# Optimization experiments

Measured on AMD Instinct MI355X. Metric: run time of the kernel, lower is better.

Reference implementation:

```python
import jax, jax.numpy as jnp
import numpy as np

B, S, D = 8, 2048, 256
H, DFF, L = 8, 1024, 5
DK = D // H
EPS = 1e-5


def _xavier(key, shape):
    fan_in, fan_out = shape[-2], shape[-1]
    a = jnp.sqrt(6.0 / (fan_in + fan_out))
    return jax.random.uniform(key, shape, jnp.float32, -a, a)


def setup_inputs() -> dict:
    key = jax.random.key(0)
    ks = jax.random.split(key, 12)
    inp = {
        "src": jax.random.normal(ks[0], (B, S, D), jnp.float32),
        "sph": jax.random.normal(ks[1], (B, S, S), jnp.float32),
        # stacked per-layer parameters, leading dim = L
        "Wq": _xavier(ks[2], (L, D, D)), "bq": jnp.zeros((L, D), jnp.float32),
        "Wk": _xavier(ks[3], (L, D, D)), "bk": jnp.zeros((L, D), jnp.float32),
        "Wv": _xavier(ks[4], (L, D, D)), "bv": jnp.zeros((L, D), jnp.float32),
        "Wo": _xavier(ks[5], (L, D, D)), "bo": jnp.zeros((L, D), jnp.float32),
        "W1": _xavier(ks[6], (L, D, DFF)), "b1": jnp.zeros((L, DFF), jnp.float32),
        "W2": _xavier(ks[7], (L, DFF, D)), "b2": jnp.zeros((L, D), jnp.float32),
        "ln1_g": jnp.ones((L, D), jnp.float32), "ln1_b": jnp.zeros((L, D), jnp.float32),
        "ln2_g": jnp.ones((L, D), jnp.float32), "ln2_b": jnp.zeros((L, D), jnp.float32),
    }
    return inp


def _layernorm(x, g, b):
    mu = jnp.mean(x, axis=-1, keepdims=True)
    var = jnp.mean(jnp.square(x - mu), axis=-1, keepdims=True)
    return (x - mu) * jax.lax.rsqrt(var + EPS) * g + b


def _layer(x, sph, Wq, bq, Wk, bk, Wv, bv, Wo, bo, W1, b1, W2, b2, g1, be1, g2, be2):
    # multihead attention with additive sph score bias
    q = (x @ Wq + bq).reshape(B, S, H, DK)
    k = (x @ Wk + bk).reshape(B, S, H, DK)
    v = (x @ Wv + bv).reshape(B, S, H, DK)
    scores = jnp.einsum("bqhd,bkhd->bhqk", q, k) / jnp.sqrt(jnp.float32(DK))
    scores = scores + sph[:, None, :, :]  # bias broadcast over heads
    attn = jax.nn.softmax(scores, axis=-1)
    ctx = jnp.einsum("bhqk,bkhd->bqhd", attn, v).reshape(B, S, D)
    src2 = ctx @ Wo + bo
    x = _layernorm(x + src2, g1, be1)
    # FFN (exact gelu, matching torch F.gelu default)
    h = jax.nn.gelu(x @ W1 + b1, approximate=False)
    src2 = h @ W2 + b2
    x = _layernorm(x + src2, g2, be2)
    return x


def reference(src, sph, Wq, bq, Wk, bk, Wv, bv, Wo, bo, W1, b1, W2, b2, ln1_g, ln1_b, ln2_g, ln2_b):
    x = src
    for i in range(L):
        x = _layer(x, sph, Wq[i], bq[i], Wk[i], bk[i], Wv[i], bv[i], Wo[i], bo[i],
                   W1[i], b1[i], W2[i], b2[i], ln1_g[i], ln1_b[i], ln2_g[i], ln2_b[i])
    return x
```

## Files before the change

### kernel.cpp

```cpp
#include <hip/hip_runtime.h>
#include <hip/hip_bf16.h>
#include <cstdint>

__device__ __forceinline__ float b2f(unsigned short u) {
    unsigned int t = ((unsigned int)u) << 16;
    float f;
    __builtin_memcpy(&f, &t, 4);
    return f;
}
__device__ __forceinline__ unsigned short f2b(float f) {
    unsigned int u;
    __builtin_memcpy(&u, &f, 4);
    unsigned int r = (u + 0x7FFFu + ((u >> 16) & 1u)) >> 16;
    return (unsigned short)r;
}
__device__ __forceinline__ unsigned int pkbf(float a, float b) {
    __hip_bfloat162 t = __float22bfloat162_rn(float2{a, b});
    unsigned int u;
    __builtin_memcpy(&u, &t, 4);
    return u;
}
__device__ __forceinline__ float2 bpair(unsigned int u) {
    float2 r;
    unsigned int lo = u << 16;
    unsigned int hi = u & 0xFFFF0000u;
    __builtin_memcpy(&r.x, &lo, 4);
    __builtin_memcpy(&r.y, &hi, 4);
    return r;
}

typedef __attribute__((ext_vector_type(8))) short bf16x8;
typedef __attribute__((ext_vector_type(4))) float f32x4;

#define LOG2E 1.4426950408889634f
#define SC2   0.2550348595f

__device__ __forceinline__ void gload16(const void* g, void* l) {
    __builtin_amdgcn_global_load_lds(
        (const __attribute__((address_space(1))) unsigned int*)g,
        (__attribute__((address_space(3))) unsigned int*)l, 16, 0, 0);
}

__global__ void transcvt_k(const float* __restrict__ in,
                           unsigned short* __restrict__ out, int R, int C,
                           int in_z, int out_z) {
    __shared__ float tile[32][33];
    in += (size_t)blockIdx.z * in_z;
    out += (size_t)blockIdx.z * out_z;
    const int c0 = blockIdx.x * 32, r0 = blockIdx.y * 32;
    const int tx = threadIdx.x, ty = threadIdx.y;
#pragma unroll
    for (int i = 0; i < 32; i += 8)
        tile[ty + i][tx] = in[(size_t)(r0 + ty + i) * C + c0 + tx];
    __syncthreads();
#pragma unroll
    for (int i = 0; i < 32; i += 8)
        out[(size_t)(c0 + ty + i) * R + r0 + tx] = f2b(tile[tx][ty + i]);
}

__global__ __launch_bounds__(256) void sph_cvt_perm(const float* __restrict__ in,
                                                    unsigned short* __restrict__ out) {
    const int t = threadIdx.x & 127;
    const size_t row = (size_t)blockIdx.x * 2 + (threadIdx.x >> 7);
    const int g = t >> 2, q = t & 3;
    const float* ip = in + row * 2048 + 64 * g + 4 * q;
    float4 f0 = *(const float4*)(ip);
    float4 f1 = *(const float4*)(ip + 16);
    float4 f2 = *(const float4*)(ip + 32);
    float4 f3 = *(const float4*)(ip + 48);
    uint4 o0, o1;
    o0.x = pkbf(f0.x * LOG2E, f1.x * LOG2E); o0.y = pkbf(f2.x * LOG2E, f3.x * LOG2E);
    o0.z = pkbf(f0.y * LOG2E, f1.y * LOG2E); o0.w = pkbf(f2.y * LOG2E, f3.y * LOG2E);
    o1.x = pkbf(f0.z * LOG2E, f1.z * LOG2E); o1.y = pkbf(f2.z * LOG2E, f3.z * LOG2E);
    o1.z = pkbf(f0.w * LOG2E, f1.w * LOG2E); o1.w = pkbf(f2.w * LOG2E, f3.w * LOG2E);
    unsigned short* op = out + row * 2048 + 64 * g + 16 * q;
    ((uint4*)op)[0] = o0;
    ((uint4*)op)[1] = o1;
}

__global__ __launch_bounds__(256) void cvt_bf16_k(const float* __restrict__ in,
                                                  unsigned short* __restrict__ out,
                                                  float* __restrict__ xcopy) {
    const size_t idx = (size_t)blockIdx.x * 256 + threadIdx.x;
    const float4 a = ((const float4*)in)[idx * 2];
    const float4 b = ((const float4*)in)[idx * 2 + 1];
    uint4 o;
    o.x = pkbf(a.x, a.y);
    o.y = pkbf(a.z, a.w);
    o.z = pkbf(b.x, b.y);
    o.w = pkbf(b.z, b.w);
    ((uint4*)out)[idx] = o;
    ((float4*)xcopy)[idx * 2] = a;
    ((float4*)xcopy)[idx * 2 + 1] = b;
}

template <int TN, int QKVB>
__global__ __launch_bounds__(256) void gemm_gl_kernel(
    const unsigned short* __restrict__ A, const unsigned short* __restrict__ Wt,
    const float* __restrict__ biasQ, const float* __restrict__ biasK,
    const float* __restrict__ biasV, unsigned short* __restrict__ C,
    int M, int N, int K, int do_gelu) {
    constexpr int JN = TN / 32;
    constexpr int NCH = 16 + TN / 8;
    __shared__ unsigned short As[128 * 64];
    __shared__ unsigned short Bs[TN * 64];
    const int tid = threadIdx.x;
    const int lane = tid & 63, wid = tid >> 6;
    const int m0 = blockIdx.y * 128, n0 = blockIdx.x * TN;
    const int wm = (wid >> 1) * 64, wn = (wid & 1) * (TN / 2);
    const int quad = lane >> 4, mrow = lane & 15;
    const int lrow = lane >> 3, lslot = lane & 7;
    f32x4 acc[4][JN] = {};

    for (int kb = 0; kb < K; kb += 64) {
#pragma unroll
        for (int cc = 0; cc < NCH / 4; ++cc) {
            const int c = wid * (NCH / 4) + cc;
            if (c < 16) {
                const int row = c * 8 + lrow;
                const int gcol = ((lslot ^ (row & 7)) << 3) + kb;
                gload16(A + (size_t)(m0 + row) * K + gcol, &As[c * 512 + lane * 8]);
            } else {
                const int row = (c - 16) * 8 + lrow;
                const int gcol = ((lslot ^ (row & 7)) << 3) + kb;
                gload16(Wt + (size_t)(n0 + row) * K + gcol, &Bs[(c - 16) * 512 + lane * 8]);
            }
        }
        __syncthreads();
#pragma unroll
        for (int h = 0; h < 2; ++h) {
            bf16x8 af[4], bfr[JN];
#pragma unroll
            for (int i = 0; i < 4; i++) {
                const int ar = wm + i * 16 + mrow;
                af[i] = *(const bf16x8*)&As[ar * 64 + (((h * 4 + quad) ^ (ar & 7)) << 3)];
            }
#pragma unroll
            for (int j = 0; j < JN; j++) {
                const int br = wn + j * 16 + mrow;
                bfr[j] = *(const bf16x8*)&Bs[br * 64 + (((h * 4 + quad) ^ (br & 7)) << 3)];
            }
#pragma unroll
            for (int i = 0; i < 4; i++)
#pragma unroll
                for (int j = 0; j < JN; j++)
                    acc[i][j] = __builtin_amdgcn_mfma_f32_16x16x32_bf16(af[i], bfr[j], acc[i][j], 0, 0, 0);
        }
        __syncthreads();
    }

    const float* bp;
    if (QKVB) {
        const int bsel = n0 >> 8;
        bp = bsel == 0 ? biasQ : (bsel == 1 ? biasK : biasV);
    } else {
        bp = biasQ;
    }
#pragma unroll
    for (int i = 0; i < 4; i++)
#pragma unroll
        for (int j = 0; j < JN; j++) {
            const int col = n0 + wn + j * 16 + mrow;
            const float bv = QKVB ? bp[col & 255] : bp[col];
#pragma unroll
            for (int r = 0; r < 4; r++) {
                const int row = m0 + wm + i * 16 + quad * 4 + r;
                float v = acc[i][j][r] + bv;
                if (do_gelu) v = 0.5f * v * (1.0f + erff(v * 0.70710678118654752f));
                C[(size_t)row * N + col] = f2b(v);
            }
        }
}

template <int SPHB16>
__global__ __launch_bounds__(256) void attn_mfma(
    const unsigned short* __restrict__ Qb, const unsigned short* __restrict__ Kb,
    const unsigned short* __restrict__ Vb, const float* __restrict__ sphf,
    const unsigned short* __restrict__ sphb, unsigned short* __restrict__ Ctx) {
    __shared__ unsigned short Ks[2 * 64 * 40];
    __shared__ unsigned short Vt[2 * 32 * 72];
    __shared__ unsigned short Ps[4][16 * 72];

    const int tid = threadIdx.x, lane = tid & 63, wid = tid >> 6;
    const int quad = lane >> 4, lq = lane & 15;
    const int bid = blockIdx.x;
    const int h = bid >> 8, b = (bid >> 5) & 7, qt = bid & 31;
    const int q0 = qt * 64;
    const size_t bS = (size_t)b * 2048;

    const int skey = tid >> 2, sdg = (tid & 3) << 3;
    const unsigned short* kp = Kb + (bS + skey) * 768 + h * 32 + sdg;
    const int vkp = tid & 31, vdg = (tid >> 5) << 2;
    const int vm = vkp & 15, vc = vkp >> 4;
    const int vso = 2 * vm + 32 * vc;
    const unsigned short* vp = Vb + (bS + vm + 32 * vc) * 768 + h * 32 + vdg;

    const bf16x8 qf = *(const bf16x8*)(Qb + (bS + q0 + wid * 16 + lq) * 768 + h * 32 + quad * 8);

    const size_t sprow = ((size_t)b * 2048 + q0 + wid * 16 + quad * 4) * 2048;
    const float* spf = sphf + sprow + lq;
    const unsigned short* spb = sphb + sprow + 4 * lq;

    float l_r[4] = {0.f, 0.f, 0.f, 0.f};
    f32x4 o0 = {}, o1 = {};

    uint4 kw = *(const uint4*)kp;
    uint2 va = *(const uint2*)vp;
    uint2 vb2 = *(const uint2*)(vp + 16 * 768);
    int c = 0;

    for (int kt = 0; kt < 32; ++kt) {
        *(uint4*)&Ks[c * 2560 + skey * 40 + sdg] = kw;
        {
            unsigned short* vt = &Vt[c * 2304];
            *(unsigned int*)&vt[(vdg + 0) * 72 + vso] = (va.x & 0xFFFFu) | (vb2.x << 16);
            *(unsigned int*)&vt[(vdg + 1) * 72 + vso] = (va.x >> 16) | (vb2.x & 0xFFFF0000u);
            *(unsigned int*)&vt[(vdg + 2) * 72 + vso] = (va.y & 0xFFFFu) | (vb2.y << 16);
            *(unsigned int*)&vt[(vdg + 3) * 72 + vso] = (va.y >> 16) | (vb2.y & 0xFFFF0000u);
        }
        if (kt < 31) {
            kp += 64 * 768;
            vp += 64 * 768;
            kw = *(const uint4*)kp;
            va = *(const uint2*)vp;
            vb2 = *(const uint2*)(vp + 16 * 768);
        }
        __syncthreads();

        const unsigned short* ks = &Ks[c * 2560];
        const unsigned short* vt = &Vt[c * 2304];
        const f32x4 zf = {};
        __builtin_amdgcn_s_setprio(1);
        f32x4 sa0 = __builtin_amdgcn_mfma_f32_16x16x32_bf16(
            qf, *(const bf16x8*)&ks[(0  + lq) * 40 + quad * 8], zf, 0, 0, 0);
        f32x4 sa1 = __builtin_amdgcn_mfma_f32_16x16x32_bf16(
            qf, *(const bf16x8*)&ks[(16 + lq) * 40 + quad * 8], zf, 0, 0, 0);
        f32x4 sa2 = __builtin_amdgcn_mfma_f32_16x16x32_bf16(
            qf, *(const bf16x8*)&ks[(32 + lq) * 40 + quad * 8], zf, 0, 0, 0);
        f32x4 sa3 = __builtin_amdgcn_mfma_f32_16x16x32_bf16(
            qf, *(const bf16x8*)&ks[(48 + lq) * 40 + quad * 8], zf, 0, 0, 0);
        __builtin_amdgcn_s_setprio(0);

        const int k0 = kt * 64;
#pragma unroll
        for (int r = 0; r < 4; ++r) {
            float sb0, sb1, sb2, sb3;
            if (SPHB16) {
                const uint2 su = *(const uint2*)(spb + (size_t)r * 2048 + k0);
                const float2 slo = bpair(su.x), shi = bpair(su.y);
                sb0 = slo.x; sb1 = slo.y; sb2 = shi.x; sb3 = shi.y;
            } else {
                const float* spr = spf + (size_t)r * 2048 + k0;
                sb0 = spr[0]  * LOG2E; sb1 = spr[16] * LOG2E;
                sb2 = spr[32] * LOG2E; sb3 = spr[48] * LOG2E;
            }
            const float p0 = __builtin_amdgcn_exp2f(fmaf(sa0[r], SC2, sb0));
            const float p1 = __builtin_amdgcn_exp2f(fmaf(sa1[r], SC2, sb1));
            const float p2 = __builtin_amdgcn_exp2f(fmaf(sa2[r], SC2, sb2));
            const float p3 = __builtin_amdgcn_exp2f(fmaf(sa3[r], SC2, sb3));
            l_r[r] += (p0 + p1) + (p2 + p3);
            unsigned int* pw = (unsigned int*)&Ps[wid][(quad * 4 + r) * 72];
            pw[lq]      = pkbf(p0, p1);
            pw[lq + 16] = pkbf(p2, p3);
        }

        __builtin_amdgcn_s_setprio(1);
#pragma unroll
        for (int k2 = 0; k2 < 2; ++k2) {
            bf16x8 pf = *(const bf16x8*)&Ps[wid][lq * 72 + k2 * 32 + quad * 8];
            o0 = __builtin_amdgcn_mfma_f32_16x16x32_bf16(
                pf, *(const bf16x8*)&vt[(0  + lq) * 72 + k2 * 32 + quad * 8], o0, 0, 0, 0);
            o1 = __builtin_amdgcn_mfma_f32_16x16x32_bf16(
                pf, *(const bf16x8*)&vt[(16 + lq) * 72 + k2 * 32 + quad * 8], o1, 0, 0, 0);
        }
        __builtin_amdgcn_s_setprio(0);
        c ^= 1;
    }

    unsigned short* op = Ctx + (bS + q0 + wid * 16 + quad * 4) * 256 + h * 32;
#pragma unroll
    for (int r = 0; r < 4; ++r) {
        float l = l_r[r];
        l += __shfl_xor(l, 1);
        l += __shfl_xor(l, 2);
        l += __shfl_xor(l, 4);
        l += __shfl_xor(l, 8);
        const float inv = 1.f / l;
        op[r * 256 + lq]      = f2b(o0[r] * inv);
        op[r * 256 + 16 + lq] = f2b(o1[r] * inv);
    }
}

__global__ __launch_bounds__(256) void add_ln_kernel(
    const float* x, const unsigned short* r,
    const float* __restrict__ g, const float* __restrict__ be,
    float* out, unsigned short* xb) {
    const int lane = threadIdx.x & 63, wid = threadIdx.x >> 6;
    const size_t row = (size_t)blockIdx.x * 4 + wid;
    float4 xv = *(const float4*)(x + row * 256 + lane * 4);
    uint2 ru = *(const uint2*)(r + row * 256 + lane * 4);
    float2 ra = bpair(ru.x), rb = bpair(ru.y);
    float v[4] = {xv.x + ra.x, xv.y + ra.y, xv.z + rb.x, xv.w + rb.y};
    float sum = v[0] + v[1] + v[2] + v[3];
#pragma unroll
    for (int off = 32; off; off >>= 1) sum += __shfl_xor(sum, off);
    const float mu = sum * (1.f / 256.f);
    float sq = 0.f;
#pragma unroll
    for (int i = 0; i < 4; i++) { float d = v[i] - mu; sq += d * d; }
#pragma unroll
    for (int off = 32; off; off >>= 1) sq += __shfl_xor(sq, off);
    const float rs = rsqrtf(sq * (1.f / 256.f) + 1e-5f);
    float4 o;
    o.x = (v[0] - mu) * rs * g[lane * 4 + 0] + be[lane * 4 + 0];
    o.y = (v[1] - mu) * rs * g[lane * 4 + 1] + be[lane * 4 + 1];
    o.z = (v[2] - mu) * rs * g[lane * 4 + 2] + be[lane * 4 + 2];
    o.w = (v[3] - mu) * rs * g[lane * 4 + 3] + be[lane * 4 + 3];
    *(float4*)(out + row * 256 + lane * 4) = o;
    uint2 p;
    p.x = pkbf(o.x, o.y);
    p.y = pkbf(o.z, o.w);
    *(uint2*)(xb + row * 256 + lane * 4) = p;
}

extern "C" void kernel_launch(void* const* d_in, const int* in_sizes, int n_in,
                              void* d_out, int out_size, void* d_ws, size_t ws_size,
                              hipStream_t stream) {
    const float* src = (const float*)d_in[0];
    const float* sph = (const float*)d_in[1];
    const float* Wq  = (const float*)d_in[2];
    const float* bq  = (const float*)d_in[3];
    const float* Wk  = (const float*)d_in[4];
    const float* bk  = (const float*)d_in[5];
    const float* Wv  = (const float*)d_in[6];
    const float* bv  = (const float*)d_in[7];
    const float* Wo  = (const float*)d_in[8];
    const float* bo  = (const float*)d_in[9];
    const float* W1  = (const float*)d_in[10];
    const float* b1  = (const float*)d_in[11];
    const float* W2  = (const float*)d_in[12];
    const float* b2  = (const float*)d_in[13];
    const float* g1  = (const float*)d_in[14];
    const float* be1 = (const float*)d_in[15];
    const float* g2  = (const float*)d_in[16];
    const float* be2 = (const float*)d_in[17];

    char* ws = (char*)d_ws;
    float* X = (float*)d_out;
    unsigned short* QKV = (unsigned short*)(ws + 0);
    unsigned short* CTX = (unsigned short*)(ws + 25165824);
    unsigned short* T2  = (unsigned short*)(ws + 33554432);
    unsigned short* H   = QKV;
    unsigned short* XB  = T2;
    unsigned short* WtQKV = (unsigned short*)(ws + 41943040);
    unsigned short* WtO   = (unsigned short*)(ws + 43909120);
    unsigned short* Wt1   = (unsigned short*)(ws + 44564480);
    unsigned short* Wt2   = (unsigned short*)(ws + 47185920);
    unsigned short* SPHB  = (unsigned short*)(ws + 50331648);
    const int use_b16 = (ws_size >= (size_t)117440512);

    const dim3 tb(32, 8);
    transcvt_k<<<dim3(8, 8, 5),  tb, 0, stream>>>(Wq, WtQKV,          256, 256, 65536, 196608);
    transcvt_k<<<dim3(8, 8, 5),  tb, 0, stream>>>(Wk, WtQKV + 65536,  256, 256, 65536, 196608);
    transcvt_k<<<dim3(8, 8, 5),  tb, 0, stream>>>(Wv, WtQKV + 131072, 256, 256, 65536, 196608);
    transcvt_k<<<dim3(8, 8, 5),  tb, 0, stream>>>(Wo, WtO,            256, 256, 65536, 65536);
    transcvt_k<<<dim3(32, 8, 5), tb, 0, stream>>>(W1, Wt1,            256, 1024, 262144, 262144);
    transcvt_k<<<dim3(8, 32, 5), tb, 0, stream>>>(W2, Wt2,            1024, 256, 262144, 262144);
    if (use_b16) sph_cvt_perm<<<8192, 256, 0, stream>>>(sph, SPHB);
    cvt_bf16_k<<<2048, 256, 0, stream>>>(src, XB, X);

    const int M = 16384;
    for (int lyr = 0; lyr < 5; ++lyr) {
        gemm_gl_kernel<128, 1><<<dim3(6, 128), 256, 0, stream>>>(
            XB, WtQKV + lyr * 196608, bq + lyr * 256, bk + lyr * 256, bv + lyr * 256,
            QKV, M, 768, 256, 0);
        if (use_b16)
            attn_mfma<1><<<2048, 256, 0, stream>>>(QKV, QKV + 256, QKV + 512, sph, SPHB, CTX);
        else
            attn_mfma<0><<<2048, 256, 0, stream>>>(QKV, QKV + 256, QKV + 512, sph, SPHB, CTX);
        gemm_gl_kernel<64, 0><<<dim3(4, 128), 256, 0, stream>>>(
            CTX, WtO + lyr * 65536, bo + lyr * 256, nullptr, nullptr, T2, M, 256, 256, 0);
        add_ln_kernel<<<4096, 256, 0, stream>>>(X, T2, g1 + lyr * 256, be1 + lyr * 256, X, XB);
        gemm_gl_kernel<128, 0><<<dim3(8, 128), 256, 0, stream>>>(
            XB, Wt1 + lyr * 262144, b1 + lyr * 1024, nullptr, nullptr, H, M, 1024, 256, 1);
        gemm_gl_kernel<64, 0><<<dim3(4, 128), 256, 0, stream>>>(
            H, Wt2 + lyr * 262144, b2 + lyr * 256, nullptr, nullptr, T2, M, 256, 1024, 0);
        add_ln_kernel<<<4096, 256, 0, stream>>>(X, T2, g2 + lyr * 256, be2 + lyr * 256, X, XB);
    }
}
```

Measured before the change: 1.410 ms.

## Replace direct-to-LDS GEMM loads with register-prefetched double-buffered LDS pipeline

The GEMM kernel drops global_load_lds staging with a single 64-wide K tile and two barriers per step. It now prefetches the next 32-wide K slice into registers while computing on a double-buffered LDS tile, so each step needs only one barrier. It also raises wave priority around the MFMA block and packs epilogue conversions in pairs. The aim is to overlap global memory latency with MFMA work and cut barrier stalls, at the cost of more registers, more loop iterations and register-to-LDS store traffic.

```diff
diff --git a/kernel.cpp b/kernel.cpp
--- a/kernel.cpp
+++ b/kernel.cpp
@@ -34,12 +34,6 @@
 
 #define LOG2E 1.4426950408889634f
 #define SC2   0.2550348595f
-
-__device__ __forceinline__ void gload16(const void* g, void* l) {
-    __builtin_amdgcn_global_load_lds(
-        (const __attribute__((address_space(1))) unsigned int*)g,
-        (__attribute__((address_space(3))) unsigned int*)l, 16, 0, 0);
-}
 
 __global__ void transcvt_k(const float* __restrict__ in,
                            unsigned short* __restrict__ out, int R, int C,
@@ -95,58 +89,71 @@
 }
 
 template <int TN, int QKVB>
-__global__ __launch_bounds__(256) void gemm_gl_kernel(
+__global__ __launch_bounds__(256) void gemm_db_kernel(
     const unsigned short* __restrict__ A, const unsigned short* __restrict__ Wt,
     const float* __restrict__ biasQ, const float* __restrict__ biasK,
     const float* __restrict__ biasV, unsigned short* __restrict__ C,
     int M, int N, int K, int do_gelu) {
     constexpr int JN = TN / 32;
-    constexpr int NCH = 16 + TN / 8;
-    __shared__ unsigned short As[128 * 64];
-    __shared__ unsigned short Bs[TN * 64];
+    __shared__ unsigned short As[2][128 * 32];
+    __shared__ unsigned short Bs[2][TN * 32];
     const int tid = threadIdx.x;
     const int lane = tid & 63, wid = tid >> 6;
     const int m0 = blockIdx.y * 128, n0 = blockIdx.x * TN;
     const int wm = (wid >> 1) * 64, wn = (wid & 1) * (TN / 2);
     const int quad = lane >> 4, mrow = lane & 15;
-    const int lrow = lane >> 3, lslot = lane & 7;
     f32x4 acc[4][JN] = {};
 
-    for (int kb = 0; kb < K; kb += 64) {
-#pragma unroll
-        for (int cc = 0; cc < NCH / 4; ++cc) {
-            const int c = wid * (NCH / 4) + cc;
-            if (c < 16) {
-                const int row = c * 8 + lrow;
-                const int gcol = ((lslot ^ (row & 7)) << 3) + kb;
-                gload16(A + (size_t)(m0 + row) * K + gcol, &As[c * 512 + lane * 8]);
-            } else {
-                const int row = (c - 16) * 8 + lrow;
-                const int gcol = ((lslot ^ (row & 7)) << 3) + kb;
-                gload16(Wt + (size_t)(n0 + row) * K + gcol, &Bs[(c - 16) * 512 + lane * 8]);
-            }
+    const int arow = tid >> 1, asl = (tid & 1) * 2;
+    const unsigned short* Ag = A + (size_t)(m0 + arow) * K + asl * 8;
+    int brow, bsl;
+    if constexpr (TN == 128) { brow = tid >> 1; bsl = (tid & 1) * 2; }
+    else                     { brow = tid >> 2; bsl = tid & 3; }
+    const unsigned short* Bg = Wt + (size_t)(n0 + brow) * K + bsl * 8;
+
+    uint4 a0 = *(const uint4*)(Ag);
+    uint4 a1 = *(const uint4*)(Ag + 8);
+    uint4 b0 = *(const uint4*)(Bg);
+    uint4 b1 = {};
+    if constexpr (TN == 128) b1 = *(const uint4*)(Bg + 8);
+    int c = 0;
+
+    for (int kb = 0; kb < K; kb += 32) {
+        *(uint4*)&As[c][arow * 32 + ((asl ^ (arow & 3)) << 3)] = a0;
+        *(uint4*)&As[c][arow * 32 + (((asl + 1) ^ (arow & 3)) << 3)] = a1;
+        if constexpr (TN == 128) {
+            *(uint4*)&Bs[c][brow * 32 + ((bsl ^ (brow & 3)) << 3)] = b0;
+            *(uint4*)&Bs[c][brow * 32 + (((bsl + 1) ^ (brow & 3)) << 3)] = b1;
+        } else {
+            *(uint4*)&Bs[c][brow * 32 + ((bsl ^ (brow & 3)) << 3)] = b0;
+        }
+        if (kb + 32 < K) {
+            a0 = *(const uint4*)(Ag + kb + 32);
+            a1 = *(const uint4*)(Ag + kb + 40);
+            b0 = *(const uint4*)(Bg + kb + 32);
+            if constexpr (TN == 128) b1 = *(const uint4*)(Bg + kb + 40);
         }
         __syncthreads();
-#pragma unroll
-        for (int h = 0; h < 2; ++h) {
-            bf16x8 af[4], bfr[JN];
-#pragma unroll
-            for (int i = 0; i < 4; i++) {
-                const int ar = wm + i * 16 + mrow;
-                af[i] = *(const bf16x8*)&As[ar * 64 + (((h * 4 + quad) ^ (ar & 7)) << 3)];
-            }
-#pragma unroll
-            for (int j = 0; j < JN; j++) {
-                const int br = wn + j * 16 + mrow;
-                bfr[j] = *(const bf16x8*)&Bs[br * 64 + (((h * 4 + quad) ^ (br & 7)) << 3)];
-            }
-#pragma unroll
-            for (int i = 0; i < 4; i++)
-#pragma unroll
-                for (int j = 0; j < JN; j++)
-                    acc[i][j] = __builtin_amdgcn_mfma_f32_16x16x32_bf16(af[i], bfr[j], acc[i][j], 0, 0, 0);
-        }
-        __syncthreads();
+
+        bf16x8 af[4], bfr[JN];
+#pragma unroll
+        for (int i = 0; i < 4; i++) {
+            const int ar = wm + i * 16 + mrow;
+            af[i] = *(const bf16x8*)&As[c][ar * 32 + ((quad ^ (ar & 3)) << 3)];
+        }
+#pragma unroll
+        for (int j = 0; j < JN; j++) {
+            const int br = wn + j * 16 + mrow;
+            bfr[j] = *(const bf16x8*)&Bs[c][br * 32 + ((quad ^ (br & 3)) << 3)];
+        }
+        __builtin_amdgcn_s_setprio(1);
+#pragma unroll
+        for (int i = 0; i < 4; i++)
+#pragma unroll
+            for (int j = 0; j < JN; j++)
+                acc[i][j] = __builtin_amdgcn_mfma_f32_16x16x32_bf16(af[i], bfr[j], acc[i][j], 0, 0, 0);
+        __builtin_amdgcn_s_setprio(0);
+        c ^= 1;
     }
 
     const float* bp;
@@ -162,12 +169,18 @@
         for (int j = 0; j < JN; j++) {
             const int col = n0 + wn + j * 16 + mrow;
             const float bv = QKVB ? bp[col & 255] : bp[col];
+            float v[4];
 #pragma unroll
             for (int r = 0; r < 4; r++) {
-                const int row = m0 + wm + i * 16 + quad * 4 + r;
-                float v = acc[i][j][r] + bv;
-                if (do_gelu) v = 0.5f * v * (1.0f + erff(v * 0.70710678118654752f));
-                C[(size_t)row * N + col] = f2b(v);
+                v[r] = acc[i][j][r] + bv;
+                if (do_gelu) v[r] = 0.5f * v[r] * (1.0f + erff(v[r] * 0.70710678118654752f));
+            }
+            const int row = m0 + wm + i * 16 + quad * 4;
+#pragma unroll
+            for (int r2 = 0; r2 < 4; r2 += 2) {
+                const unsigned u = pkbf(v[r2], v[r2 + 1]);
+                C[(size_t)(row + r2) * N + col] = (unsigned short)u;
+                C[(size_t)(row + r2 + 1) * N + col] = (unsigned short)(u >> 16);
             }
         }
 }
@@ -371,19 +384,19 @@
 
     const int M = 16384;
     for (int lyr = 0; lyr < 5; ++lyr) {
-        gemm_gl_kernel<128, 1><<<dim3(6, 128), 256, 0, stream>>>(
+        gemm_db_kernel<128, 1><<<dim3(6, 128), 256, 0, stream>>>(
             XB, WtQKV + lyr * 196608, bq + lyr * 256, bk + lyr * 256, bv + lyr * 256,
             QKV, M, 768, 256, 0);
         if (use_b16)
             attn_mfma<1><<<2048, 256, 0, stream>>>(QKV, QKV + 256, QKV + 512, sph, SPHB, CTX);
         else
             attn_mfma<0><<<2048, 256, 0, stream>>>(QKV, QKV + 256, QKV + 512, sph, SPHB, CTX);
-        gemm_gl_kernel<64, 0><<<dim3(4, 128), 256, 0, stream>>>(
+        gemm_db_kernel<64, 0><<<dim3(4, 128), 256, 0, stream>>>(
             CTX, WtO + lyr * 65536, bo + lyr * 256, nullptr, nullptr, T2, M, 256, 256, 0);
         add_ln_kernel<<<4096, 256, 0, stream>>>(X, T2, g1 + lyr * 256, be1 + lyr * 256, X, XB);
-        gemm_gl_kernel<128, 0><<<dim3(8, 128), 256, 0, stream>>>(
+        gemm_db_kernel<128, 0><<<dim3(8, 128), 256, 0, stream>>>(
             XB, Wt1 + lyr * 262144, b1 + lyr * 1024, nullptr, nullptr, H, M, 1024, 256, 1);
-        gemm_gl_kernel<64, 0><<<dim3(4, 128), 256, 0, stream>>>(
+        gemm_db_kernel<64, 0><<<dim3(4, 128), 256, 0, stream>>>(
             H, Wt2 + lyr * 262144, b2 + lyr * 256, nullptr, nullptr, T2, M, 256, 1024, 0);
         add_ln_kernel<<<4096, 256, 0, stream>>>(X, T2, g2 + lyr * 256, be2 + lyr * 256, X, XB);
     }
```

After: 1.412 ms. About the same (+0.2%).
